# Kernel optimization log

Measured on AMD Instinct MI355X. Metric: run time of the kernel, lower is better.

## Reference

```python
import jax, jax.numpy as jnp
import numpy as np

B, S, D = 32, 2048, 1024
MASK_PENALTY = 100000000.0

def setup_inputs() -> dict:
    key = jax.random.key(0)
    k1, k2, k3 = jax.random.split(key, 3)
    target_t = jax.random.normal(k1, (B, D), dtype=jnp.float32)
    context = jax.random.normal(k2, (B, S, D), dtype=jnp.float32)
    context_mask = jax.random.randint(k3, (B, S), 0, 2).astype(jnp.float32)
    # ensure at least one valid position per row to avoid all -1e8 softmax
    context_mask = context_mask.at[:, 0].set(1.0)
    return {"target_t": target_t, "context": context, "context_mask": context_mask}

def reference(target_t, context, context_mask):
    # scores: [B,S] = batched dot of each context row with the single query
    atten = jnp.einsum('bsd,bd->bs', context, target_t)
    atten = atten + (context_mask - 1.0) * MASK_PENALTY
    atten = jax.nn.softmax(atten, axis=1)
    # weighted sum of context rows: [B,D]
    context_combined = jnp.einsum('bs,bsd->bd', atten, context)
    return context_combined
```

## Files before the change

### kernel.cpp

```cpp
#include <hip/hip_runtime.h>
#include <math.h>

#define BD 32
#define SD 2048
#define DD 1024
#define MASK_PENALTY 100000000.0f
#define RR 8
#define NTHREADS 256

__global__ __launch_bounds__(NTHREADS) void attn_partial(
    const float* __restrict__ target,
    const float* __restrict__ context,
    const float* __restrict__ mask,
    float* __restrict__ wsO,
    float* __restrict__ wsM,
    float* __restrict__ wsL,
    int C)
{
    const int g = blockIdx.x;
    const int b = g / C;
    const int c = g % C;
    const int rows = SD / C;
    const int s0 = c * rows;
    const int t = threadIdx.x;
    const int lane = t & 63;
    const int wave = t >> 6;

    __shared__ float s_part[2][4][RR];
    __shared__ float s_sc[2][RR];

    const float4 tgt = *(const float4*)(target + (size_t)b * DD + t * 4);
    const float* ctx = context + ((size_t)b * SD + s0) * DD + t * 4;
    const float* mk  = mask + (size_t)b * SD + s0;

    float4 o = make_float4(0.f, 0.f, 0.f, 0.f);
    float m = -INFINITY;
    float l = 0.f;

    for (int i = 0; i < rows; i += RR) {
        const int buf = (i / RR) & 1;
        float4 x[RR];
        float part[RR];
        #pragma unroll
        for (int r = 0; r < RR; ++r)
            x[r] = *(const float4*)(ctx + (size_t)(i + r) * DD);
        #pragma unroll
        for (int r = 0; r < RR; ++r)
            part[r] = x[r].x * tgt.x + x[r].y * tgt.y + x[r].z * tgt.z + x[r].w * tgt.w;
        #pragma unroll
        for (int r = 0; r < RR; ++r) {
            #pragma unroll
            for (int off = 32; off > 0; off >>= 1)
                part[r] += __shfl_xor(part[r], off);
        }
        if (lane == 0) {
            #pragma unroll
            for (int r = 0; r < RR; ++r) s_part[buf][wave][r] = part[r];
        }
        __syncthreads();
        if (t < RR) {
            float sc = s_part[buf][0][t] + s_part[buf][1][t] +
                       s_part[buf][2][t] + s_part[buf][3][t];
            sc += (mk[i + t] - 1.0f) * MASK_PENALTY;
            s_sc[buf][t] = sc;
        }
        __syncthreads();
        float sc[RR];
        float mnew = m;
        #pragma unroll
        for (int r = 0; r < RR; ++r) { sc[r] = s_sc[buf][r]; mnew = fmaxf(mnew, sc[r]); }
        const float alpha = __expf(m - mnew);
        float p[RR];
        float psum = 0.f;
        #pragma unroll
        for (int r = 0; r < RR; ++r) { p[r] = __expf(sc[r] - mnew); psum += p[r]; }
        l = l * alpha + psum;
        o.x *= alpha; o.y *= alpha; o.z *= alpha; o.w *= alpha;
        #pragma unroll
        for (int r = 0; r < RR; ++r) {
            o.x += p[r] * x[r].x; o.y += p[r] * x[r].y;
            o.z += p[r] * x[r].z; o.w += p[r] * x[r].w;
        }
        m = mnew;
    }

    *(float4*)(wsO + (size_t)g * DD + t * 4) = o;
    if (t == 0) { wsM[g] = m; wsL[g] = l; }
}

__global__ __launch_bounds__(NTHREADS) void attn_combine(
    const float* __restrict__ wsO,
    const float* __restrict__ wsM,
    const float* __restrict__ wsL,
    float* __restrict__ out,
    int C)
{
    const int b = blockIdx.x;
    const int t = threadIdx.x;
    __shared__ float w[64];

    if (t < 64) {
        float mv = (t < C) ? wsM[b * C + t] : -INFINITY;
        float mred = mv;
        #pragma unroll
        for (int off = 32; off > 0; off >>= 1)
            mred = fmaxf(mred, __shfl_xor(mred, off));
        float lw = (t < C) ? wsL[b * C + t] * __expf(mv - mred) : 0.f;
        float lsum = lw;
        #pragma unroll
        for (int off = 32; off > 0; off >>= 1)
            lsum += __shfl_xor(lsum, off);
        w[t] = (t < C) ? __expf(mv - mred) / lsum : 0.f;
    }
    __syncthreads();

    float4 acc = make_float4(0.f, 0.f, 0.f, 0.f);
    for (int c = 0; c < C; ++c) {
        float4 v = *(const float4*)(wsO + ((size_t)(b * C + c)) * DD + t * 4);
        float wc = w[c];
        acc.x += wc * v.x; acc.y += wc * v.y; acc.z += wc * v.z; acc.w += wc * v.w;
    }
    *(float4*)(out + (size_t)b * DD + t * 4) = acc;
}

extern "C" void kernel_launch(void* const* d_in, const int* in_sizes, int n_in,
                              void* d_out, int out_size, void* d_ws, size_t ws_size,
                              hipStream_t stream) {
    const float* target  = (const float*)d_in[0];
    const float* context = (const float*)d_in[1];
    const float* mask    = (const float*)d_in[2];
    float* out = (float*)d_out;

    int C = 32;
    while (C > 1 && (size_t)BD * C * (DD + 2) * sizeof(float) > ws_size) C >>= 1;

    float* wsO = (float*)d_ws;
    float* wsM = wsO + (size_t)BD * C * DD;
    float* wsL = wsM + (size_t)BD * C;

    attn_partial<<<BD * C, NTHREADS, 0, stream>>>(target, context, mask, wsO, wsM, wsL, C);
    attn_combine<<<BD, NTHREADS, 0, stream>>>(wsO, wsM, wsL, out, C);
}
```

Before: 366.1 us.

## Give each wave its own rows to remove per-chunk block barriers

Each wave now takes a contiguous quarter of the block's rows and handles full 1024-wide rows, so the dot product reduces within a wave by shuffles. This removes the two __syncthreads per 8-row chunk and the shared-memory score exchange. The four waves' online-softmax states are merged through 16KB of shared memory at the end, and launch bounds now request 4 blocks per CU. The trade-off is less memory-level parallelism per wave (2 rows in flight instead of 8 per block), plus higher register and LDS use.

```diff
diff --git a/kernel.cpp b/kernel.cpp
--- a/kernel.cpp
+++ b/kernel.cpp
@@ -5,10 +5,11 @@
 #define SD 2048
 #define DD 1024
 #define MASK_PENALTY 100000000.0f
-#define RR 8
 #define NTHREADS 256
+#define NW 4
+#define UR 2
 
-__global__ __launch_bounds__(NTHREADS) void attn_partial(
+__global__ __launch_bounds__(NTHREADS, 4) void attn_partial(
     const float* __restrict__ target,
     const float* __restrict__ context,
     const float* __restrict__ mask,
@@ -24,68 +25,101 @@
     const int s0 = c * rows;
     const int t = threadIdx.x;
     const int lane = t & 63;
-    const int wave = t >> 6;
+    const int w = t >> 6;
 
-    __shared__ float s_part[2][4][RR];
-    __shared__ float s_sc[2][RR];
+    float4 tgt[4];
+    #pragma unroll
+    for (int j = 0; j < 4; ++j)
+        tgt[j] = *(const float4*)(target + (size_t)b * DD + j * 256 + lane * 4);
 
-    const float4 tgt = *(const float4*)(target + (size_t)b * DD + t * 4);
-    const float* ctx = context + ((size_t)b * SD + s0) * DD + t * 4;
-    const float* mk  = mask + (size_t)b * SD + s0;
+    const int rpw = rows / NW;
+    const int r0 = w * rpw;
+    const float* ctx = context + ((size_t)b * SD + s0 + r0) * DD + lane * 4;
+    const float* mk  = mask + (size_t)b * SD + s0 + r0;
 
-    float4 o = make_float4(0.f, 0.f, 0.f, 0.f);
-    float m = -INFINITY;
-    float l = 0.f;
+    float4 o[4];
+    #pragma unroll
+    for (int j = 0; j < 4; ++j) o[j] = make_float4(0.f, 0.f, 0.f, 0.f);
+    float m = -INFINITY, l = 0.f;
 
-    for (int i = 0; i < rows; i += RR) {
-        const int buf = (i / RR) & 1;
-        float4 x[RR];
-        float part[RR];
+    for (int i = 0; i < rpw; i += UR) {
+        float4 x[UR][4];
         #pragma unroll
-        for (int r = 0; r < RR; ++r)
-            x[r] = *(const float4*)(ctx + (size_t)(i + r) * DD);
+        for (int r = 0; r < UR; ++r) {
+            const float* rp = ctx + (size_t)(i + r) * DD;
+            #pragma unroll
+            for (int j = 0; j < 4; ++j)
+                x[r][j] = *(const float4*)(rp + j * 256);
+        }
+        float sc[UR];
         #pragma unroll
-        for (int r = 0; r < RR; ++r)
-            part[r] = x[r].x * tgt.x + x[r].y * tgt.y + x[r].z * tgt.z + x[r].w * tgt.w;
+        for (int r = 0; r < UR; ++r) {
+            float s = 0.f;
+            #pragma unroll
+            for (int j = 0; j < 4; ++j) {
+                s = fmaf(x[r][j].x, tgt[j].x, s);
+                s = fmaf(x[r][j].y, tgt[j].y, s);
+                s = fmaf(x[r][j].z, tgt[j].z, s);
+                s = fmaf(x[r][j].w, tgt[j].w, s);
+            }
+            sc[r] = s;
+        }
         #pragma unroll
-        for (int r = 0; r < RR; ++r) {
+        for (int off = 32; off > 0; off >>= 1) {
             #pragma unroll
-            for (int off = 32; off > 0; off >>= 1)
-                part[r] += __shfl_xor(part[r], off);
+            for (int r = 0; r < UR; ++r)
+                sc[r] += __shfl_xor(sc[r], off);
         }
-        if (lane == 0) {
-            #pragma unroll
-            for (int r = 0; r < RR; ++r) s_part[buf][wave][r] = part[r];
-        }
-        __syncthreads();
-        if (t < RR) {
-            float sc = s_part[buf][0][t] + s_part[buf][1][t] +
-                       s_part[buf][2][t] + s_part[buf][3][t];
-            sc += (mk[i + t] - 1.0f) * MASK_PENALTY;
-            s_sc[buf][t] = sc;
-        }
-        __syncthreads();
-        float sc[RR];
+        #pragma unroll
+        for (int r = 0; r < UR; ++r)
+            sc[r] += (mk[i + r] - 1.0f) * MASK_PENALTY;
+
         float mnew = m;
         #pragma unroll
-        for (int r = 0; r < RR; ++r) { sc[r] = s_sc[buf][r]; mnew = fmaxf(mnew, sc[r]); }
+        for (int r = 0; r < UR; ++r) mnew = fmaxf(mnew, sc[r]);
         const float alpha = __expf(m - mnew);
-        float p[RR];
-        float psum = 0.f;
+        float p[UR], ps = 0.f;
         #pragma unroll
-        for (int r = 0; r < RR; ++r) { p[r] = __expf(sc[r] - mnew); psum += p[r]; }
-        l = l * alpha + psum;
-        o.x *= alpha; o.y *= alpha; o.z *= alpha; o.w *= alpha;
+        for (int r = 0; r < UR; ++r) { p[r] = __expf(sc[r] - mnew); ps += p[r]; }
+        l = l * alpha + ps;
         #pragma unroll
-        for (int r = 0; r < RR; ++r) {
-            o.x += p[r] * x[r].x; o.y += p[r] * x[r].y;
-            o.z += p[r] * x[r].z; o.w += p[r] * x[r].w;
+        for (int j = 0; j < 4; ++j) {
+            o[j].x *= alpha; o[j].y *= alpha; o[j].z *= alpha; o[j].w *= alpha;
+            #pragma unroll
+            for (int r = 0; r < UR; ++r) {
+                o[j].x = fmaf(p[r], x[r][j].x, o[j].x);
+                o[j].y = fmaf(p[r], x[r][j].y, o[j].y);
+                o[j].z = fmaf(p[r], x[r][j].z, o[j].z);
+                o[j].w = fmaf(p[r], x[r][j].w, o[j].w);
+            }
         }
         m = mnew;
     }
 
-    *(float4*)(wsO + (size_t)g * DD + t * 4) = o;
-    if (t == 0) { wsM[g] = m; wsL[g] = l; }
+    __shared__ float sM[NW];
+    __shared__ float sL[NW];
+    __shared__ float sO[NW][DD];
+    if (lane == 0) { sM[w] = m; sL[w] = l; }
+    __syncthreads();
+    float M = fmaxf(fmaxf(sM[0], sM[1]), fmaxf(sM[2], sM[3]));
+    float lsum = 0.f;
+    #pragma unroll
+    for (int ww = 0; ww < NW; ++ww) lsum += sL[ww] * __expf(sM[ww] - M);
+    const float aw = __expf(m - M);
+    #pragma unroll
+    for (int j = 0; j < 4; ++j) {
+        float4 v = make_float4(o[j].x * aw, o[j].y * aw, o[j].z * aw, o[j].w * aw);
+        *(float4*)(&sO[w][j * 256 + lane * 4]) = v;
+    }
+    __syncthreads();
+    float4 acc = make_float4(0.f, 0.f, 0.f, 0.f);
+    #pragma unroll
+    for (int ww = 0; ww < NW; ++ww) {
+        float4 v = *(const float4*)(&sO[ww][t * 4]);
+        acc.x += v.x; acc.y += v.y; acc.z += v.z; acc.w += v.w;
+    }
+    *(float4*)(wsO + (size_t)g * DD + t * 4) = acc;
+    if (t == 0) { wsM[g] = M; wsL[g] = lsum; }
 }
 
 __global__ __launch_bounds__(NTHREADS) void attn_combine(
@@ -97,7 +131,7 @@
 {
     const int b = blockIdx.x;
     const int t = threadIdx.x;
-    __shared__ float w[64];
+    __shared__ float wgt[64];
 
     if (t < 64) {
         float mv = (t < C) ? wsM[b * C + t] : -INFINITY;
@@ -110,15 +144,16 @@
         #pragma unroll
         for (int off = 32; off > 0; off >>= 1)
             lsum += __shfl_xor(lsum, off);
-        w[t] = (t < C) ? __expf(mv - mred) / lsum : 0.f;
+        wgt[t] = (t < C) ? __expf(mv - mred) / lsum : 0.f;
     }
     __syncthreads();
 
     float4 acc = make_float4(0.f, 0.f, 0.f, 0.f);
     for (int c = 0; c < C; ++c) {
         float4 v = *(const float4*)(wsO + ((size_t)(b * C + c)) * DD + t * 4);
-        float wc = w[c];
-        acc.x += wc * v.x; acc.y += wc * v.y; acc.z += wc * v.z; acc.w += wc * v.w;
+        float wc = wgt[c];
+        acc.x = fmaf(wc, v.x, acc.x); acc.y = fmaf(wc, v.y, acc.y);
+        acc.z = fmaf(wc, v.z, acc.z); acc.w = fmaf(wc, v.w, acc.w);
     }
     *(float4*)(out + (size_t)b * DD + t * 4) = acc;
 }
```

Result: no change. 367.3 us (+0.3%).
